# Optimization experiments

Hardware: AMD Instinct MI355X
Metric: run time of the kernel (lower is better)

The kernel has to match this reference:

```python
import jax, jax.numpy as jnp
import numpy as np

IN_DIM = 512
ATT_DIM = 64
B, N = 4, 4096


def setup_inputs() -> dict:
    key = jax.random.key(0)
    k1, k2, k3, k4 = jax.random.split(key, 4)
    x = jax.random.normal(k1, (B, N, IN_DIM), dtype=jnp.float32)
    adj_matrix = (jax.random.uniform(k2, (B, N, N)) < 0.05).astype(jnp.float32)
    # nn.Linear weights: qk_nn (2*att_dim, in_dim), v_nn (in_dim, in_dim), no bias
    W_qk = jax.random.normal(k3, (2 * ATT_DIM, IN_DIM), dtype=jnp.float32) / np.sqrt(IN_DIM)
    W_v = jax.random.normal(k4, (IN_DIM, IN_DIM), dtype=jnp.float32) / np.sqrt(IN_DIM)
    return {"x": x, "adj_matrix": adj_matrix, "W_qk": W_qk, "W_v": W_v}


def reference(x, adj_matrix, W_qk, W_v):
    # q, k: (B, N, att_dim) from a single fused projection, then chunk
    qk = jnp.einsum('bnd,ed->bne', x, W_qk)
    q, k = jnp.split(qk, 2, axis=-1)
    v = jnp.einsum('bnd,ed->bne', x, W_v)  # (B, N, in_dim)
    inv_scale = 1.0 / (ATT_DIM ** 0.5)
    # dense NxN scores masked by adjacency, row-summed -> (B, N, 1)
    scores = jnp.einsum('bnd,bmd->bnm', q, k) * inv_scale
    w = jnp.sum(scores * adj_matrix, axis=-1, keepdims=True)
    w = jax.nn.softmax(w, axis=1)  # softmax over bag dimension N
    return w * v
```

## Files before the change

kernel.cpp:

```cpp
#include <hip/hip_runtime.h>
#include <hip/hip_bf16.h>

#define B_   4
#define N_   4096
#define IND  512
#define ATT  64
#define QKD  128

#define KSPLIT 4
#define KCHUNK 1024

typedef __attribute__((ext_vector_type(8))) short short8v;
typedef __attribute__((ext_vector_type(4))) float f32x4;

__global__ __launch_bounds__(256)
void gemm_nt_f32(const float* __restrict__ X, const float* __restrict__ W,
                 float* __restrict__ C, int M, int K, int Nout) {
  __shared__ __align__(16) float Xs[32][68];
  __shared__ __align__(16) float Ws[32][68];
  const int tid = threadIdx.x;
  const int tx = tid & 15, ty = tid >> 4;
  const int m0 = blockIdx.x * 64, n0 = blockIdx.y * 64;

  float acc[4][4] = {};

  for (int k0 = 0; k0 < K; k0 += 32) {
    for (int f = tid; f < 512; f += 256) {
      const int r = f >> 3;
      const int c4 = (f & 7) << 2;
      const float4 vx = *(const float4*)(X + (size_t)(m0 + r) * K + k0 + c4);
      Xs[c4 + 0][r] = vx.x; Xs[c4 + 1][r] = vx.y;
      Xs[c4 + 2][r] = vx.z; Xs[c4 + 3][r] = vx.w;
      const float4 vw = *(const float4*)(W + (size_t)(n0 + r) * K + k0 + c4);
      Ws[c4 + 0][r] = vw.x; Ws[c4 + 1][r] = vw.y;
      Ws[c4 + 2][r] = vw.z; Ws[c4 + 3][r] = vw.w;
    }
    __syncthreads();

#pragma unroll
    for (int kk = 0; kk < 32; ++kk) {
      const float4 a = *(const float4*)&Xs[kk][ty << 2];
      const float4 b = *(const float4*)&Ws[kk][tx << 2];
      const float av[4] = {a.x, a.y, a.z, a.w};
      const float bv[4] = {b.x, b.y, b.z, b.w};
#pragma unroll
      for (int i = 0; i < 4; ++i)
#pragma unroll
        for (int j = 0; j < 4; ++j) acc[i][j] += av[i] * bv[j];
    }
    __syncthreads();
  }

#pragma unroll
  for (int i = 0; i < 4; ++i) {
    float4 o = make_float4(acc[i][0], acc[i][1], acc[i][2], acc[i][3]);
    *(float4*)(C + (size_t)(m0 + (ty << 2) + i) * Nout + n0 + (tx << 2)) = o;
  }
}

__global__ __launch_bounds__(256)
void prep_k(const float* __restrict__ qk, unsigned short* __restrict__ ktf) {
  __shared__ unsigned short sh[32][68];
  __shared__ unsigned short sl[32][68];
  const int b    = blockIdx.x >> 7;
  const int slab = blockIdx.x & 127;
  const int t = threadIdx.x;

#pragma unroll
  for (int i = 0; i < 2; ++i) {
    const int f = t + i * 256;
    const int ml  = f >> 4;
    const int ch4 = (f & 15) << 2;
    const float4 v = *(const float4*)(qk +
        ((size_t)b * N_ + slab * 32 + ml) * QKD + ATT + ch4);
    const float vv[4] = {v.x, v.y, v.z, v.w};
#pragma unroll
    for (int j = 0; j < 4; ++j) {
      const unsigned short hi = (unsigned short)(__float_as_uint(vv[j]) >> 16);
      const float fhi = __uint_as_float((unsigned)hi << 16);
      const unsigned short lo = (unsigned short)(__float_as_uint(vv[j] - fhi) >> 16);
      sh[ml][ch4 + j] = hi;
      sl[ml][ch4 + j] = lo;
    }
  }
  __syncthreads();

  const int lane = t & 63;
  const int c    = t >> 6;
  const int mb   = (lane >> 4) << 3;
  const int ch   = c * 16 + (lane & 15);
  unsigned short* outb = ktf +
      (((size_t)(b * 128 + slab) * 4 + c) * 2) * 512 + (size_t)lane * 8;
  union { short8v v; unsigned short u[8]; } hv, lv;
#pragma unroll
  for (int j = 0; j < 8; ++j) {
    hv.u[j] = sh[mb + j][ch];
    lv.u[j] = sl[mb + j][ch];
  }
  *(short8v*)(outb)       = hv.v;
  *(short8v*)(outb + 512) = lv.v;
}

__global__ __launch_bounds__(256)
void adjk_mfma(const float* __restrict__ adj,
               const unsigned short* __restrict__ ktf,
               float* __restrict__ kapart) {
  const int lane = threadIdx.x & 63;
  const int wid  = threadIdx.x >> 6;
  const int g0   = blockIdx.x * 64 + wid * 16;
  const int b    = g0 >> 12;
  const int split = blockIdx.y;
  const int k0   = split * KCHUNK;
  const int slab0 = k0 >> 5;

  const int arow = lane & 15;
  const int koff = (lane >> 4) << 3;

  const float* aptr = adj + (size_t)(g0 + arow) * N_ + k0 + koff;
  const unsigned short* kbase =
      ktf + (size_t)(b * 128 + slab0) * 4096 + (size_t)lane * 8;

  f32x4 acc[4] = {{0.f,0.f,0.f,0.f},{0.f,0.f,0.f,0.f},
                  {0.f,0.f,0.f,0.f},{0.f,0.f,0.f,0.f}};

  float4 a0 = *(const float4*)(aptr);
  float4 a1 = *(const float4*)(aptr + 4);

  for (int s = 0; s < 32; ++s) {
    const unsigned short* kb = kbase + (size_t)s * 4096;
    const short8v b00 = *(const short8v*)(kb);
    const short8v b01 = *(const short8v*)(kb + 512);
    const short8v b10 = *(const short8v*)(kb + 1024);
    const short8v b11 = *(const short8v*)(kb + 1536);
    const short8v b20 = *(const short8v*)(kb + 2048);
    const short8v b21 = *(const short8v*)(kb + 2560);
    const short8v b30 = *(const short8v*)(kb + 3072);
    const short8v b31 = *(const short8v*)(kb + 3584);

    const int sn = (s < 31) ? s + 1 : 31;
    const float4 n0 = *(const float4*)(aptr + sn * 32);
    const float4 n1 = *(const float4*)(aptr + sn * 32 + 4);

    union { short8v v; unsigned short u[8]; } af;
    const float av[8] = {a0.x, a0.y, a0.z, a0.w, a1.x, a1.y, a1.z, a1.w};
#pragma unroll
    for (int j = 0; j < 8; ++j)
      af.u[j] = (unsigned short)(__float_as_uint(av[j]) >> 16);

    acc[0] = __builtin_amdgcn_mfma_f32_16x16x32_bf16(af.v, b00, acc[0], 0, 0, 0);
    acc[0] = __builtin_amdgcn_mfma_f32_16x16x32_bf16(af.v, b01, acc[0], 0, 0, 0);
    acc[1] = __builtin_amdgcn_mfma_f32_16x16x32_bf16(af.v, b10, acc[1], 0, 0, 0);
    acc[1] = __builtin_amdgcn_mfma_f32_16x16x32_bf16(af.v, b11, acc[1], 0, 0, 0);
    acc[2] = __builtin_amdgcn_mfma_f32_16x16x32_bf16(af.v, b20, acc[2], 0, 0, 0);
    acc[2] = __builtin_amdgcn_mfma_f32_16x16x32_bf16(af.v, b21, acc[2], 0, 0, 0);
    acc[3] = __builtin_amdgcn_mfma_f32_16x16x32_bf16(af.v, b30, acc[3], 0, 0, 0);
    acc[3] = __builtin_amdgcn_mfma_f32_16x16x32_bf16(af.v, b31, acc[3], 0, 0, 0);

    a0 = n0; a1 = n1;
  }

  float* outp = kapart +
      ((size_t)split * (B_ * N_) + g0 + ((lane >> 4) << 2)) * ATT + (lane & 15);
#pragma unroll
  for (int c = 0; c < 4; ++c)
#pragma unroll
    for (int r = 0; r < 4; ++r)
      outp[(size_t)r * ATT + c * 16] = acc[c][r];
}

__global__ __launch_bounds__(256)
void qdot(const float* __restrict__ qk, const float* __restrict__ kapart,
          float* __restrict__ wpre) {
  const int wid  = threadIdx.x >> 6;
  const int lane = threadIdx.x & 63;
  const int row  = blockIdx.x * 4 + wid;

  float ka = 0.f;
#pragma unroll
  for (int s = 0; s < KSPLIT; ++s)
    ka += kapart[((size_t)s * B_ * N_ + row) * ATT + lane];

  const float q = qk[(size_t)row * QKD + lane];
  float val = q * ka;
#pragma unroll
  for (int off = 32; off; off >>= 1) val += __shfl_xor(val, off);
  if (lane == 0) wpre[row] = val * 0.125f;
}

__global__ __launch_bounds__(256)
void softmax_bag(float* __restrict__ w) {
  __shared__ float red[256];
  const int b = blockIdx.x;
  float* wb = w + (size_t)b * N_;
  const int t = threadIdx.x;

  float vals[16];
  float mx = -1e30f;
#pragma unroll
  for (int i = 0; i < 16; ++i) {
    vals[i] = wb[t + i * 256];
    mx = fmaxf(mx, vals[i]);
  }
  red[t] = mx; __syncthreads();
  for (int s = 128; s; s >>= 1) {
    if (t < s) red[t] = fmaxf(red[t], red[t + s]);
    __syncthreads();
  }
  mx = red[0];
  __syncthreads();

  float sum = 0.f;
#pragma unroll
  for (int i = 0; i < 16; ++i) {
    vals[i] = expf(vals[i] - mx);
    sum += vals[i];
  }
  red[t] = sum; __syncthreads();
  for (int s = 128; s; s >>= 1) {
    if (t < s) red[t] += red[t + s];
    __syncthreads();
  }
  const float inv = 1.f / red[0];
#pragma unroll
  for (int i = 0; i < 16; ++i) wb[t + i * 256] = vals[i] * inv;
}

__global__ __launch_bounds__(256)
void scale_v(float* __restrict__ out, const float* __restrict__ w, int total4) {
  int idx = blockIdx.x * blockDim.x + threadIdx.x;
  const int stride = gridDim.x * blockDim.x;
  for (; idx < total4; idx += stride) {
    float4 v = ((const float4*)out)[idx];
    const float s = w[idx >> 7];
    v.x *= s; v.y *= s; v.z *= s; v.w *= s;
    ((float4*)out)[idx] = v;
  }
}

extern "C" void kernel_launch(void* const* d_in, const int* in_sizes, int n_in,
                              void* d_out, int out_size, void* d_ws, size_t ws_size,
                              hipStream_t stream) {
  const float* x    = (const float*)d_in[0];
  const float* adj  = (const float*)d_in[1];
  const float* W_qk = (const float*)d_in[2];
  const float* W_v  = (const float*)d_in[3];
  float* out = (float*)d_out;

  float* qk     = (float*)d_ws;
  float* kapart = qk + (size_t)B_ * N_ * QKD;
  float* wpre   = kapart + (size_t)KSPLIT * B_ * N_ * ATT;
  unsigned short* ktf = (unsigned short*)(wpre + B_ * N_);

  const int M = B_ * N_;

  {
    dim3 grid(M / 64, IND / 64);
    gemm_nt_f32<<<grid, 256, 0, stream>>>(x, W_v, out, M, IND, IND);
  }
  {
    dim3 grid(M / 64, QKD / 64);
    gemm_nt_f32<<<grid, 256, 0, stream>>>(x, W_qk, qk, M, IND, QKD);
  }
  prep_k<<<B_ * 128, 256, 0, stream>>>(qk, ktf);
  {
    dim3 grid(M / 64, KSPLIT);
    adjk_mfma<<<grid, 256, 0, stream>>>(adj, ktf, kapart);
  }
  qdot<<<M / 4, 256, 0, stream>>>(qk, kapart, wpre);
  softmax_bag<<<B_, 256, 0, stream>>>(wpre);
  const int total4 = M * (IND / 4);
  scale_v<<<2048, 256, 0, stream>>>(out, wpre, total4);
}
```

Baseline: 603.8 us.

## Replace fp32 SIMT projection GEMMs with split-bf16 MFMA and widen adjk tiles

The scalar fp32 tiled GEMMs for the V and QK projections are replaced by MFMA bf16 GEMMs. Inputs and weights are pre-split into hi/lo bf16 fragment layouts, and three MFMAs per step (hi*hi, lo*hi, hi*lo) keep near-fp32 accuracy. Separately, adjk_mfma now handles two 16-row tiles per wave so each loaded K fragment is reused twice, and its launch bounds are raised for occupancy. The cost is extra prep kernels and workspace traffic to write the fragment-layout copies of x and the weights.

```diff
diff --git a/kernel.cpp b/kernel.cpp
--- a/kernel.cpp
+++ b/kernel.cpp
@@ -13,49 +13,82 @@
 typedef __attribute__((ext_vector_type(8))) short short8v;
 typedef __attribute__((ext_vector_type(4))) float f32x4;
 
-__global__ __launch_bounds__(256)
-void gemm_nt_f32(const float* __restrict__ X, const float* __restrict__ W,
-                 float* __restrict__ C, int M, int K, int Nout) {
-  __shared__ __align__(16) float Xs[32][68];
-  __shared__ __align__(16) float Ws[32][68];
-  const int tid = threadIdx.x;
-  const int tx = tid & 15, ty = tid >> 4;
-  const int m0 = blockIdx.x * 64, n0 = blockIdx.y * 64;
-
-  float acc[4][4] = {};
-
-  for (int k0 = 0; k0 < K; k0 += 32) {
-    for (int f = tid; f < 512; f += 256) {
-      const int r = f >> 3;
-      const int c4 = (f & 7) << 2;
-      const float4 vx = *(const float4*)(X + (size_t)(m0 + r) * K + k0 + c4);
-      Xs[c4 + 0][r] = vx.x; Xs[c4 + 1][r] = vx.y;
-      Xs[c4 + 2][r] = vx.z; Xs[c4 + 3][r] = vx.w;
-      const float4 vw = *(const float4*)(W + (size_t)(n0 + r) * K + k0 + c4);
-      Ws[c4 + 0][r] = vw.x; Ws[c4 + 1][r] = vw.y;
-      Ws[c4 + 2][r] = vw.z; Ws[c4 + 3][r] = vw.w;
+__device__ __forceinline__ void f8_to_bf16_hilo(const float4& v0, const float4& v1,
+                                                short8v& hi, short8v& lo) {
+  union { short8v v; unsigned short u[8]; } h, l;
+  const float av[8] = {v0.x, v0.y, v0.z, v0.w, v1.x, v1.y, v1.z, v1.w};
+#pragma unroll
+  for (int j = 0; j < 8; ++j) {
+    const unsigned short hu = (unsigned short)(__float_as_uint(av[j]) >> 16);
+    const float fh = __uint_as_float((unsigned)hu << 16);
+    h.u[j] = hu;
+    l.u[j] = (unsigned short)(__float_as_uint(av[j] - fh) >> 16);
+  }
+  hi = h.v; lo = l.v;
+}
+
+__global__ __launch_bounds__(256)
+void prep_frag(const float* __restrict__ src, unsigned short* __restrict__ dst,
+               int nct) {
+  const int wid = threadIdx.x >> 6, lane = threadIdx.x & 63;
+  const int ct = blockIdx.x * 4 + wid;
+  if (ct >= nct) return;
+  const float* s = src + ((size_t)ct * 16 + (lane & 15)) * IND + ((lane >> 4) << 3);
+  unsigned short* d = dst + (size_t)ct * 16 * 2 * 512 + (size_t)lane * 8;
+#pragma unroll 4
+  for (int slab = 0; slab < 16; ++slab) {
+    const float4 v0 = *(const float4*)(s + slab * 32);
+    const float4 v1 = *(const float4*)(s + slab * 32 + 4);
+    short8v hv, lv;
+    f8_to_bf16_hilo(v0, v1, hv, lv);
+    *(short8v*)(d + (size_t)slab * 2 * 512)       = hv;
+    *(short8v*)(d + (size_t)slab * 2 * 512 + 512) = lv;
+  }
+}
+
+__global__ __launch_bounds__(256, 2)
+void gemm_mfma(const unsigned short* __restrict__ xf,
+               const unsigned short* __restrict__ wf,
+               float* __restrict__ C, int Nout) {
+  const int lane = threadIdx.x & 63;
+  const int wid  = threadIdx.x >> 6;
+  const int g0   = blockIdx.x * 64 + wid * 16;
+  const int mt   = g0 >> 4;
+  const int ct0  = blockIdx.y * 8;
+
+  const unsigned short* xb = xf + (size_t)mt * 16 * 2 * 512 + (size_t)lane * 8;
+  const unsigned short* wb = wf + (size_t)ct0 * 16 * 2 * 512 + (size_t)lane * 8;
+
+  f32x4 acc[8] = {{0.f,0.f,0.f,0.f},{0.f,0.f,0.f,0.f},{0.f,0.f,0.f,0.f},
+                  {0.f,0.f,0.f,0.f},{0.f,0.f,0.f,0.f},{0.f,0.f,0.f,0.f},
+                  {0.f,0.f,0.f,0.f},{0.f,0.f,0.f,0.f}};
+
+  short8v axh = *(const short8v*)(xb);
+  short8v axl = *(const short8v*)(xb + 512);
+
+  for (int slab = 0; slab < 16; ++slab) {
+    const int sn = (slab < 15) ? slab + 1 : 15;
+    const short8v nxh = *(const short8v*)(xb + (size_t)sn * 1024);
+    const short8v nxl = *(const short8v*)(xb + (size_t)sn * 1024 + 512);
+
+#pragma unroll
+    for (int c = 0; c < 8; ++c) {
+      const unsigned short* wp = wb + ((size_t)(c * 16 + slab) * 2) * 512;
+      const short8v bh = *(const short8v*)(wp);
+      const short8v bl = *(const short8v*)(wp + 512);
+      acc[c] = __builtin_amdgcn_mfma_f32_16x16x32_bf16(axh, bh, acc[c], 0, 0, 0);
+      acc[c] = __builtin_amdgcn_mfma_f32_16x16x32_bf16(axl, bh, acc[c], 0, 0, 0);
+      acc[c] = __builtin_amdgcn_mfma_f32_16x16x32_bf16(axh, bl, acc[c], 0, 0, 0);
     }
-    __syncthreads();
-
-#pragma unroll
-    for (int kk = 0; kk < 32; ++kk) {
-      const float4 a = *(const float4*)&Xs[kk][ty << 2];
-      const float4 b = *(const float4*)&Ws[kk][tx << 2];
-      const float av[4] = {a.x, a.y, a.z, a.w};
-      const float bv[4] = {b.x, b.y, b.z, b.w};
-#pragma unroll
-      for (int i = 0; i < 4; ++i)
-#pragma unroll
-        for (int j = 0; j < 4; ++j) acc[i][j] += av[i] * bv[j];
-    }
-    __syncthreads();
-  }
-
-#pragma unroll
-  for (int i = 0; i < 4; ++i) {
-    float4 o = make_float4(acc[i][0], acc[i][1], acc[i][2], acc[i][3]);
-    *(float4*)(C + (size_t)(m0 + (ty << 2) + i) * Nout + n0 + (tx << 2)) = o;
-  }
+    axh = nxh; axl = nxl;
+  }
+
+  float* outp = C + ((size_t)g0 + ((lane >> 4) << 2)) * Nout + ct0 * 16 + (lane & 15);
+#pragma unroll
+  for (int c = 0; c < 8; ++c)
+#pragma unroll
+    for (int r = 0; r < 4; ++r)
+      outp[(size_t)r * Nout + c * 16] = acc[c][r];
 }
 
 __global__ __launch_bounds__(256)
@@ -101,13 +134,13 @@
   *(short8v*)(outb + 512) = lv.v;
 }
 
-__global__ __launch_bounds__(256)
+__global__ __launch_bounds__(256, 2)
 void adjk_mfma(const float* __restrict__ adj,
                const unsigned short* __restrict__ ktf,
                float* __restrict__ kapart) {
   const int lane = threadIdx.x & 63;
   const int wid  = threadIdx.x >> 6;
-  const int g0   = blockIdx.x * 64 + wid * 16;
+  const int g0   = blockIdx.x * 128 + wid * 32;
   const int b    = g0 >> 12;
   const int split = blockIdx.y;
   const int k0   = split * KCHUNK;
@@ -116,15 +149,20 @@
   const int arow = lane & 15;
   const int koff = (lane >> 4) << 3;
 
-  const float* aptr = adj + (size_t)(g0 + arow) * N_ + k0 + koff;
+  const float* aptr0 = adj + (size_t)(g0 + arow) * N_ + k0 + koff;
+  const float* aptr1 = aptr0 + (size_t)16 * N_;
   const unsigned short* kbase =
       ktf + (size_t)(b * 128 + slab0) * 4096 + (size_t)lane * 8;
 
-  f32x4 acc[4] = {{0.f,0.f,0.f,0.f},{0.f,0.f,0.f,0.f},
-                  {0.f,0.f,0.f,0.f},{0.f,0.f,0.f,0.f}};
-
-  float4 a0 = *(const float4*)(aptr);
-  float4 a1 = *(const float4*)(aptr + 4);
+  f32x4 acc[2][4] = {{{0.f,0.f,0.f,0.f},{0.f,0.f,0.f,0.f},
+                      {0.f,0.f,0.f,0.f},{0.f,0.f,0.f,0.f}},
+                     {{0.f,0.f,0.f,0.f},{0.f,0.f,0.f,0.f},
+                      {0.f,0.f,0.f,0.f},{0.f,0.f,0.f,0.f}}};
+
+  float4 a00 = *(const float4*)(aptr0);
+  float4 a01 = *(const float4*)(aptr0 + 4);
+  float4 a10 = *(const float4*)(aptr1);
+  float4 a11 = *(const float4*)(aptr1 + 4);
 
   for (int s = 0; s < 32; ++s) {
     const unsigned short* kb = kbase + (size_t)s * 4096;
@@ -138,34 +176,53 @@
     const short8v b31 = *(const short8v*)(kb + 3584);
 
     const int sn = (s < 31) ? s + 1 : 31;
-    const float4 n0 = *(const float4*)(aptr + sn * 32);
-    const float4 n1 = *(const float4*)(aptr + sn * 32 + 4);
-
-    union { short8v v; unsigned short u[8]; } af;
-    const float av[8] = {a0.x, a0.y, a0.z, a0.w, a1.x, a1.y, a1.z, a1.w};
-#pragma unroll
-    for (int j = 0; j < 8; ++j)
-      af.u[j] = (unsigned short)(__float_as_uint(av[j]) >> 16);
-
-    acc[0] = __builtin_amdgcn_mfma_f32_16x16x32_bf16(af.v, b00, acc[0], 0, 0, 0);
-    acc[0] = __builtin_amdgcn_mfma_f32_16x16x32_bf16(af.v, b01, acc[0], 0, 0, 0);
-    acc[1] = __builtin_amdgcn_mfma_f32_16x16x32_bf16(af.v, b10, acc[1], 0, 0, 0);
-    acc[1] = __builtin_amdgcn_mfma_f32_16x16x32_bf16(af.v, b11, acc[1], 0, 0, 0);
-    acc[2] = __builtin_amdgcn_mfma_f32_16x16x32_bf16(af.v, b20, acc[2], 0, 0, 0);
-    acc[2] = __builtin_amdgcn_mfma_f32_16x16x32_bf16(af.v, b21, acc[2], 0, 0, 0);
-    acc[3] = __builtin_amdgcn_mfma_f32_16x16x32_bf16(af.v, b30, acc[3], 0, 0, 0);
-    acc[3] = __builtin_amdgcn_mfma_f32_16x16x32_bf16(af.v, b31, acc[3], 0, 0, 0);
-
-    a0 = n0; a1 = n1;
-  }
-
-  float* outp = kapart +
-      ((size_t)split * (B_ * N_) + g0 + ((lane >> 4) << 2)) * ATT + (lane & 15);
-#pragma unroll
-  for (int c = 0; c < 4; ++c)
-#pragma unroll
-    for (int r = 0; r < 4; ++r)
-      outp[(size_t)r * ATT + c * 16] = acc[c][r];
+    const float4 n00 = *(const float4*)(aptr0 + sn * 32);
+    const float4 n01 = *(const float4*)(aptr0 + sn * 32 + 4);
+    const float4 n10 = *(const float4*)(aptr1 + sn * 32);
+    const float4 n11 = *(const float4*)(aptr1 + sn * 32 + 4);
+
+    union { short8v v; unsigned short u[8]; } af0, af1;
+    {
+      const float av0[8] = {a00.x,a00.y,a00.z,a00.w,a01.x,a01.y,a01.z,a01.w};
+      const float av1[8] = {a10.x,a10.y,a10.z,a10.w,a11.x,a11.y,a11.z,a11.w};
+#pragma unroll
+      for (int j = 0; j < 8; ++j) {
+        af0.u[j] = (unsigned short)(__float_as_uint(av0[j]) >> 16);
+        af1.u[j] = (unsigned short)(__float_as_uint(av1[j]) >> 16);
+      }
+    }
+
+    acc[0][0] = __builtin_amdgcn_mfma_f32_16x16x32_bf16(af0.v, b00, acc[0][0], 0,0,0);
+    acc[0][0] = __builtin_amdgcn_mfma_f32_16x16x32_bf16(af0.v, b01, acc[0][0], 0,0,0);
+    acc[0][1] = __builtin_amdgcn_mfma_f32_16x16x32_bf16(af0.v, b10, acc[0][1], 0,0,0);
+    acc[0][1] = __builtin_amdgcn_mfma_f32_16x16x32_bf16(af0.v, b11, acc[0][1], 0,0,0);
+    acc[0][2] = __builtin_amdgcn_mfma_f32_16x16x32_bf16(af0.v, b20, acc[0][2], 0,0,0);
+    acc[0][2] = __builtin_amdgcn_mfma_f32_16x16x32_bf16(af0.v, b21, acc[0][2], 0,0,0);
+    acc[0][3] = __builtin_amdgcn_mfma_f32_16x16x32_bf16(af0.v, b30, acc[0][3], 0,0,0);
+    acc[0][3] = __builtin_amdgcn_mfma_f32_16x16x32_bf16(af0.v, b31, acc[0][3], 0,0,0);
+    acc[1][0] = __builtin_amdgcn_mfma_f32_16x16x32_bf16(af1.v, b00, acc[1][0], 0,0,0);
+    acc[1][0] = __builtin_amdgcn_mfma_f32_16x16x32_bf16(af1.v, b01, acc[1][0], 0,0,0);
+    acc[1][1] = __builtin_amdgcn_mfma_f32_16x16x32_bf16(af1.v, b10, acc[1][1], 0,0,0);
+    acc[1][1] = __builtin_amdgcn_mfma_f32_16x16x32_bf16(af1.v, b11, acc[1][1], 0,0,0);
+    acc[1][2] = __builtin_amdgcn_mfma_f32_16x16x32_bf16(af1.v, b20, acc[1][2], 0,0,0);
+    acc[1][2] = __builtin_amdgcn_mfma_f32_16x16x32_bf16(af1.v, b21, acc[1][2], 0,0,0);
+    acc[1][3] = __builtin_amdgcn_mfma_f32_16x16x32_bf16(af1.v, b30, acc[1][3], 0,0,0);
+    acc[1][3] = __builtin_amdgcn_mfma_f32_16x16x32_bf16(af1.v, b31, acc[1][3], 0,0,0);
+
+    a00 = n00; a01 = n01; a10 = n10; a11 = n11;
+  }
+
+#pragma unroll
+  for (int tile = 0; tile < 2; ++tile) {
+    float* outp = kapart +
+        ((size_t)split * (B_ * N_) + g0 + tile * 16 + ((lane >> 4) << 2)) * ATT
+        + (lane & 15);
+#pragma unroll
+    for (int c = 0; c < 4; ++c)
+#pragma unroll
+      for (int r = 0; r < 4; ++r)
+        outp[(size_t)r * ATT + c * 16] = acc[tile][c][r];
+  }
 }
 
 __global__ __launch_bounds__(256)
@@ -249,21 +306,28 @@
   float* qk     = (float*)d_ws;
   float* kapart = qk + (size_t)B_ * N_ * QKD;
   float* wpre   = kapart + (size_t)KSPLIT * B_ * N_ * ATT;
-  unsigned short* ktf = (unsigned short*)(wpre + B_ * N_);
+  unsigned short* ktf  = (unsigned short*)(wpre + B_ * N_);
+  unsigned short* xft  = ktf + (size_t)B_ * 128 * 4096;
+  unsigned short* wvf  = xft + (size_t)1024 * 16 * 2 * 512;
+  unsigned short* wqkf = wvf + (size_t)32 * 16 * 2 * 512;
 
   const int M = B_ * N_;
 
+  prep_frag<<<256, 256, 0, stream>>>(x, xft, 1024);
+  prep_frag<<<8, 256, 0, stream>>>(W_v, wvf, 32);
+  prep_frag<<<2, 256, 0, stream>>>(W_qk, wqkf, 8);
+
   {
-    dim3 grid(M / 64, IND / 64);
-    gemm_nt_f32<<<grid, 256, 0, stream>>>(x, W_v, out, M, IND, IND);
+    dim3 grid(M / 64, QKD / 128);
+    gemm_mfma<<<grid, 256, 0, stream>>>(xft, wqkf, qk, QKD);
   }
   {
-    dim3 grid(M / 64, QKD / 64);
-    gemm_nt_f32<<<grid, 256, 0, stream>>>(x, W_qk, qk, M, IND, QKD);
+    dim3 grid(M / 64, IND / 128);
+    gemm_mfma<<<grid, 256, 0, stream>>>(xft, wvf, out, IND);
   }
   prep_k<<<B_ * 128, 256, 0, stream>>>(qk, ktf);
   {
-    dim3 grid(M / 64, KSPLIT);
+    dim3 grid(M / 128, KSPLIT);
     adjk_mfma<<<grid, 256, 0, stream>>>(adj, ktf, kapart);
   }
   qdot<<<M / 4, 256, 0, stream>>>(qk, kapart, wpre);
```

After: 518.9 us. -14.0%, faster.
